# Kernel optimization log

Measured on AMD Instinct MI355X. Metric: run time of the kernel, lower is better.

## Reference

```python
import jax, jax.numpy as jnp
import numpy as np

B, N, DIM = 2, 2048, 1024
HEADS, DIM_HEAD = 16, 64
INNER = HEADS * DIM_HEAD  # 1024
SCALE = DIM_HEAD ** -0.5


def setup_inputs() -> dict:
    key = jax.random.key(0)
    ks = jax.random.split(key, 8)
    s = DIM ** -0.5
    return {
        "x1": jax.random.normal(ks[0], (B, N, DIM), jnp.float32),
        "x2": jax.random.normal(ks[1], (B, N, DIM), jnp.float32),
        "W_qkv1": jax.random.normal(ks[2], (DIM, INNER * 3), jnp.float32) * s,
        "W_qkv2": jax.random.normal(ks[3], (DIM, INNER * 3), jnp.float32) * s,
        "W_out1": jax.random.normal(ks[4], (INNER, DIM), jnp.float32) * s,
        "b_out1": jnp.zeros((DIM,), jnp.float32),
        "W_out2": jax.random.normal(ks[5], (INNER, DIM), jnp.float32) * s,
        "b_out2": jnp.zeros((DIM,), jnp.float32),
    }


def _split_heads(t):
    # [b, n, (h d)] -> [b, h, n, d]
    b, n, _ = t.shape
    return t.reshape(b, n, HEADS, DIM_HEAD).transpose(0, 2, 1, 3)


def _merge_heads(t):
    # [b, h, n, d] -> [b, n, (h d)]
    b, h, n, d = t.shape
    return t.transpose(0, 2, 1, 3).reshape(b, n, h * d)


def reference(x1, x2, W_qkv1, W_qkv2, W_out1, b_out1, W_out2, b_out2):
    qkv1 = x1 @ W_qkv1  # [b, n, 3*inner]
    qkv2 = x2 @ W_qkv2
    q1, k1, v1 = [_split_heads(t) for t in jnp.split(qkv1, 3, axis=-1)]
    q2, k2, v2 = [_split_heads(t) for t in jnp.split(qkv2, 3, axis=-1)]

    # direction 1: queries from stream 2 attend to keys/values of stream 1
    dots1 = jnp.einsum('bhid,bhjd->bhij', q2, k1) * SCALE
    attn1 = jax.nn.softmax(dots1, axis=-1)
    out1 = jnp.einsum('bhij,bhjd->bhid', attn1, v1)
    out1 = _merge_heads(out1) @ W_out1 + b_out1

    # direction 2: queries from stream 1 attend to keys/values of stream 2
    dots2 = jnp.einsum('bhid,bhjd->bhij', q1, k2) * SCALE
    attn2 = jax.nn.softmax(dots2, axis=-1)
    out2 = jnp.einsum('bhij,bhjd->bhid', attn2, v2)
    out2 = _merge_heads(out2) @ W_out2 + b_out2

    return (out1, out2)
```

## Files before the change

### kernel.cpp

```cpp
#include <hip/hip_runtime.h>

typedef __attribute__((ext_vector_type(8))) short short8;
typedef __attribute__((ext_vector_type(4))) float f32x4;
typedef __attribute__((ext_vector_type(16))) float f32x16;
using u16 = unsigned short;

#define DEV static __device__ __forceinline__
#define SCL 0.18033688011112042f

DEV u16 f2bf(float f) {
  union { float f; unsigned u; } v; v.f = f;
  unsigned r = v.u + 0x7FFFu + ((v.u >> 16) & 1u);
  return (u16)(r >> 16);
}

DEV unsigned cvtpk(float lo, float hi_) {
  unsigned d;
  asm("v_cvt_pk_bf16_f32 %0, %1, %2" : "=v"(d) : "v"(lo), "v"(hi_));
  return d;
}

DEV void gld16(const void* g, void* l) {
  __builtin_amdgcn_global_load_lds(
      (const __attribute__((address_space(1))) unsigned*)g,
      (__attribute__((address_space(3))) unsigned*)l, 16, 0, 0);
}

__global__ __launch_bounds__(256) void conv_f32_bf16(const float* __restrict__ s0,
                                                     const float* __restrict__ s1,
                                                     u16* __restrict__ d0,
                                                     u16* __restrict__ d1, int n8) {
  const float* src = blockIdx.z ? s1 : s0;
  u16* dst = blockIdx.z ? d1 : d0;
  int i = blockIdx.x * 256 + threadIdx.x;
  if (i >= n8) return;
  const float4* s = reinterpret_cast<const float4*>(src) + (size_t)i * 2;
  float4 a = s[0], b = s[1];
  union { u16 s[8]; uint4 v; } t;
  t.s[0]=f2bf(a.x); t.s[1]=f2bf(a.y); t.s[2]=f2bf(a.z); t.s[3]=f2bf(a.w);
  t.s[4]=f2bf(b.x); t.s[5]=f2bf(b.y); t.s[6]=f2bf(b.z); t.s[7]=f2bf(b.w);
  reinterpret_cast<uint4*>(dst)[i] = t.v;
}

__global__ __launch_bounds__(256) void transpose_w(const float* __restrict__ s0,
                                                   const float* __restrict__ s1,
                                                   u16* __restrict__ d0,
                                                   u16* __restrict__ d1, int R, int C,
                                                   int qcols, float qscale) {
  const float* src = blockIdx.z ? s1 : s0;
  u16* dst = blockIdx.z ? d1 : d0;
  __shared__ float tile[32][33];
  int tx = threadIdx.x & 31, ty = threadIdx.x >> 5;
  int rb = blockIdx.y * 32, cb = blockIdx.x * 32;
#pragma unroll
  for (int j = 0; j < 32; j += 8)
    tile[ty + j][tx] = src[(size_t)(rb + ty + j) * C + cb + tx];
  __syncthreads();
#pragma unroll
  for (int j = 0; j < 32; j += 8) {
    int c = cb + ty + j;
    float sc = (c < qcols) ? qscale : 1.0f;
    dst[(size_t)c * R + rb + tx] = f2bf(tile[tx][ty + j] * sc);
  }
}

__global__ __launch_bounds__(256) void gemm_bt(
    const u16* __restrict__ A0, const u16* __restrict__ A1,
    const u16* __restrict__ B0, const u16* __restrict__ B1,
    u16* __restrict__ Cb0, u16* __restrict__ Cb1,
    float* __restrict__ Cf0, float* __restrict__ Cf1,
    const float* __restrict__ bias0, const float* __restrict__ bias1,
    int M, int N, int K) {
  const int z = blockIdx.z;
  const u16* A  = z ? A1 : A0;
  const u16* Bt = z ? B1 : B0;
  u16* Cb = z ? Cb1 : Cb0;
  float* Cf = z ? Cf1 : Cf0;
  const float* bias = z ? bias1 : bias0;

  __shared__ __align__(16) char smem[32768];
  char* As = smem;
  char* Bs = smem + 16384;
  const int tid = threadIdx.x;
  const int lane = tid & 63, wave = tid >> 6;
  const int wm = wave >> 1, wn = wave & 1;
  const int lr = lane & 15, lk = lane >> 4;
  const size_t m0 = (size_t)blockIdx.x * 128, n0 = (size_t)blockIdx.y * 128;

  f32x4 acc[4][4] = {};

  for (int k0 = 0; k0 < K; k0 += 64) {
    __syncthreads();
#pragma unroll
    for (int i = 0; i < 4; ++i) {
      int idx = tid + i * 256;
      int r = idx >> 3, c = idx & 7;
      int cs = c ^ (r & 7);
      gld16(A + (m0 + r) * (size_t)K + k0 + cs * 8, As + idx * 16);
    }
#pragma unroll
    for (int i = 0; i < 4; ++i) {
      int idx = tid + i * 256;
      int r = idx >> 3, c = idx & 7;
      int cs = c ^ (r & 7);
      gld16(Bt + (n0 + r) * (size_t)K + k0 + cs * 8, Bs + idx * 16);
    }
    __syncthreads();
#pragma unroll
    for (int kk = 0; kk < 2; ++kk) {
      short8 af[4], bfr[4];
#pragma unroll
      for (int mf = 0; mf < 4; ++mf) {
        int r = wm * 64 + mf * 16 + lr;
        af[mf] = *reinterpret_cast<const short8*>(As + r * 128 + (((kk * 4 + lk) ^ (r & 7)) * 16));
      }
#pragma unroll
      for (int nf = 0; nf < 4; ++nf) {
        int r = wn * 64 + nf * 16 + lr;
        bfr[nf] = *reinterpret_cast<const short8*>(Bs + r * 128 + (((kk * 4 + lk) ^ (r & 7)) * 16));
      }
#pragma unroll
      for (int mf = 0; mf < 4; ++mf)
#pragma unroll
        for (int nf = 0; nf < 4; ++nf)
          acc[mf][nf] = __builtin_amdgcn_mfma_f32_16x16x32_bf16(af[mf], bfr[nf], acc[mf][nf], 0, 0, 0);
    }
  }
  const int row0 = (int)m0 + wm * 64, col0 = (int)n0 + wn * 64;
  if (Cf) {
#pragma unroll
    for (int nf = 0; nf < 4; ++nf) {
      int col = col0 + nf * 16 + lr;
      float bv = bias ? bias[col] : 0.0f;
#pragma unroll
      for (int mf = 0; mf < 4; ++mf)
#pragma unroll
        for (int g = 0; g < 4; ++g) {
          int row = row0 + mf * 16 + lk * 4 + g;
          Cf[(size_t)row * N + col] = acc[mf][nf][g] + bv;
        }
    }
  } else {
#pragma unroll
    for (int nf = 0; nf < 4; ++nf) {
      int col = col0 + nf * 16 + lr;
#pragma unroll
      for (int mf = 0; mf < 4; ++mf)
#pragma unroll
        for (int g = 0; g < 4; ++g) {
          int row = row0 + mf * 16 + lk * 4 + g;
          Cb[(size_t)row * N + col] = f2bf(acc[mf][nf][g]);
        }
    }
  }
}

__global__ __launch_bounds__(256) void vtrans(const u16* __restrict__ q0,
                                              const u16* __restrict__ q1,
                                              u16* __restrict__ v0p,
                                              u16* __restrict__ v1p) {
  const u16* qkv = blockIdx.z ? q1 : q0;
  u16* vT = blockIdx.z ? v1p : v0p;
  __shared__ u16 tile[64][72];
  int t = threadIdx.x;
  int bh = blockIdx.y;
  int b = bh >> 4, h = bh & 15;
  int n0 = blockIdx.x * 64;
  int n = t >> 2, dc = t & 3;
  const u16* src = qkv + (size_t)(b * 2048 + n0 + n) * 3072 + 2048 + h * 64 + dc * 16;
  uint4 w0 = *reinterpret_cast<const uint4*>(src);
  uint4 w1 = *reinterpret_cast<const uint4*>(src + 8);
  *reinterpret_cast<uint4*>(&tile[n][dc * 16]) = w0;
  *reinterpret_cast<uint4*>(&tile[n][dc * 16 + 8]) = w1;
  __syncthreads();
  int d = t >> 2, nc = t & 3;
  union { u16 s[8]; uint4 v; } o0, o1;
#pragma unroll
  for (int j = 0; j < 8; ++j) { o0.s[j] = tile[nc * 16 + j][d]; o1.s[j] = tile[nc * 16 + 8 + j][d]; }
  u16* dst = vT + ((size_t)(bh * 64 + d)) * 2048 + n0 + nc * 16;
  *reinterpret_cast<uint4*>(dst) = o0.v;
  *reinterpret_cast<uint4*>(dst + 8) = o1.v;
}

#define KOFF0 0
#define VOFF0 (8192 + 64)
#define KOFF1 (16384 + 128)
#define VOFF1 (KOFF1 + 8192 + 64)

__global__ __launch_bounds__(256, 2) void flash(
    const u16* __restrict__ qkv1, const u16* __restrict__ qkv2,
    const u16* __restrict__ vT1, const u16* __restrict__ vT2,
    u16* __restrict__ ao1, u16* __restrict__ ao2) {
  const int bid = blockIdx.x;
  const int bh_dir = bid & 63;
  const int qt = bid >> 6;
  const int dir = bh_dir >> 5;
  const int bh = bh_dir & 31;
  const int b = bh >> 4, h = bh & 15;
  const u16* qkvQ  = dir ? qkv1 : qkv2;
  const u16* qkvKV = dir ? qkv2 : qkv1;
  const u16* vT    = dir ? vT2 : vT1;
  u16* Oout        = dir ? ao2 : ao1;

  __shared__ __align__(16) char smem[33024];

  const int tid = threadIdx.x;
  const int lane = tid & 63, wave = tid >> 6;
  const int l31 = lane & 31, hi = lane >> 5;

  const int qbase = qt * 256 + wave * 64;
  const u16* qp0 = qkvQ + (size_t)(b * 2048 + qbase + l31) * 3072 + h * 64 + hi * 8;
  const u16* qp1 = qp0 + (size_t)32 * 3072;
  short8 qf0[4], qf1[4];
#pragma unroll
  for (int c = 0; c < 4; ++c) {
    qf0[c] = *reinterpret_cast<const short8*>(qp0 + c * 16);
    qf1[c] = *reinterpret_cast<const short8*>(qp1 + c * 16);
  }

  auto STAGE = [&](char* kb, char* vb, int kv0) {
#pragma unroll
    for (int i = 0; i < 2; ++i) {
      int idx = tid + i * 256;
      int r = idx >> 3, c = idx & 7, cs = c ^ (r & 7);
      gld16(qkvKV + (size_t)(b * 2048 + kv0 + r) * 3072 + 1024 + h * 64 + cs * 8, kb + idx * 16);
      gld16(vT + (size_t)(bh * 64 + r) * 2048 + kv0 + cs * 8, vb + idx * 16);
    }
  };

  short8 ones;
#pragma unroll
  for (int j = 0; j < 8; ++j) ones[j] = (short)0x3F80;

  f32x16 oA0 = {}, oA1 = {}, oB0 = {}, oB1 = {}, laccA = {}, laccB = {};

  STAGE(smem + KOFF0, smem + VOFF0, 0);

  union U8 { unsigned u[4]; short8 s8; };

  for (int t = 0; t < 32; ++t) {
    char* Ks = smem + ((t & 1) ? KOFF1 : KOFF0);
    char* Vs = smem + ((t & 1) ? VOFF1 : VOFF0);
    __syncthreads();
    if (t < 31)
      STAGE(smem + ((t & 1) ? KOFF0 : KOFF1), smem + ((t & 1) ? VOFF0 : VOFF1), (t + 1) * 64);

    short8 kf[8];
#pragma unroll
    for (int c = 0; c < 4; ++c) {
      int sw = ((c * 2 + hi) ^ (l31 & 7)) * 16;
      kf[c]     = *reinterpret_cast<const short8*>(Ks + l31 * 128 + sw);
      kf[c + 4] = *reinterpret_cast<const short8*>(Ks + (32 + l31) * 128 + sw);
    }

    f32x16 sA0 = {}, sA1 = {};
#pragma unroll
    for (int c = 0; c < 4; ++c) {
      sA0 = __builtin_amdgcn_mfma_f32_32x32x16_bf16(kf[c],     qf0[c], sA0, 0, 0, 0);
      sA1 = __builtin_amdgcn_mfma_f32_32x32x16_bf16(kf[c + 4], qf0[c], sA1, 0, 0, 0);
    }
#pragma unroll
    for (int r = 0; r < 16; ++r) sA0[r] = __builtin_exp2f(sA0[r]);
#pragma unroll
    for (int r = 0; r < 16; ++r) sA1[r] = __builtin_exp2f(sA1[r]);
    short8 paA[4];
#pragma unroll
    for (int kc = 0; kc < 4; ++kc) {
      const f32x16& S = (kc < 2) ? sA0 : sA1;
      int rb = (kc & 1) * 8;
      unsigned a0 = cvtpk(S[rb + 0], S[rb + 1]);
      unsigned b0 = cvtpk(S[rb + 4], S[rb + 5]);
      asm volatile("v_permlane32_swap_b32 %0, %1" : "+v"(a0), "+v"(b0));
      unsigned a1 = cvtpk(S[rb + 2], S[rb + 3]);
      unsigned b1 = cvtpk(S[rb + 6], S[rb + 7]);
      asm volatile("v_permlane32_swap_b32 %0, %1" : "+v"(a1), "+v"(b1));
      U8 u; u.u[0] = a0; u.u[1] = a1; u.u[2] = b0; u.u[3] = b1;
      paA[kc] = u.s8;
    }

    f32x16 sB0 = {}, sB1 = {};
#pragma unroll
    for (int c = 0; c < 4; ++c) {
      sB0 = __builtin_amdgcn_mfma_f32_32x32x16_bf16(kf[c],     qf1[c], sB0, 0, 0, 0);
      sB1 = __builtin_amdgcn_mfma_f32_32x32x16_bf16(kf[c + 4], qf1[c], sB1, 0, 0, 0);
    }

    short8 vf[8];
#pragma unroll
    for (int kc = 0; kc < 4; ++kc) {
      int sw = ((kc * 2 + hi) ^ (l31 & 7)) * 16;
      vf[kc]     = *reinterpret_cast<const short8*>(Vs + l31 * 128 + sw);
      vf[kc + 4] = *reinterpret_cast<const short8*>(Vs + (32 + l31) * 128 + sw);
    }

#pragma unroll
    for (int r = 0; r < 16; ++r) sB0[r] = __builtin_exp2f(sB0[r]);
#pragma unroll
    for (int r = 0; r < 16; ++r) sB1[r] = __builtin_exp2f(sB1[r]);
    short8 paB[4];
#pragma unroll
    for (int kc = 0; kc < 4; ++kc) {
      const f32x16& S = (kc < 2) ? sB0 : sB1;
      int rb = (kc & 1) * 8;
      unsigned a0 = cvtpk(S[rb + 0], S[rb + 1]);
      unsigned b0 = cvtpk(S[rb + 4], S[rb + 5]);
      asm volatile("v_permlane32_swap_b32 %0, %1" : "+v"(a0), "+v"(b0));
      unsigned a1 = cvtpk(S[rb + 2], S[rb + 3]);
      unsigned b1 = cvtpk(S[rb + 6], S[rb + 7]);
      asm volatile("v_permlane32_swap_b32 %0, %1" : "+v"(a1), "+v"(b1));
      U8 u; u.u[0] = a0; u.u[1] = a1; u.u[2] = b0; u.u[3] = b1;
      paB[kc] = u.s8;
    }

#pragma unroll
    for (int kc = 0; kc < 4; ++kc) {
      oA0 = __builtin_amdgcn_mfma_f32_32x32x16_bf16(paA[kc], vf[kc],     oA0, 0, 0, 0);
      oA1 = __builtin_amdgcn_mfma_f32_32x32x16_bf16(paA[kc], vf[kc + 4], oA1, 0, 0, 0);
      oB0 = __builtin_amdgcn_mfma_f32_32x32x16_bf16(paB[kc], vf[kc],     oB0, 0, 0, 0);
      oB1 = __builtin_amdgcn_mfma_f32_32x32x16_bf16(paB[kc], vf[kc + 4], oB1, 0, 0, 0);
      laccA = __builtin_amdgcn_mfma_f32_32x32x16_bf16(paA[kc], ones, laccA, 0, 0, 0);
      laccB = __builtin_amdgcn_mfma_f32_32x32x16_bf16(paB[kc], ones, laccB, 0, 0, 0);
    }
  }

  const int rowbase = b * 2048 + qt * 256 + wave * 64;
#pragma unroll
  for (int r = 0; r < 16; ++r) {
    int q = (r & 3) + 8 * (r >> 2) + 4 * hi;
    float liA = 1.0f / laccA[r], liB = 1.0f / laccB[r];
    u16* opA = Oout + (size_t)(rowbase + q) * 1024 + h * 64 + l31;
    u16* opB = opA + (size_t)32 * 1024;
    opA[0]  = f2bf(oA0[r] * liA);
    opA[32] = f2bf(oA1[r] * liA);
    opB[0]  = f2bf(oB0[r] * liB);
    opB[32] = f2bf(oB1[r] * liB);
  }
}

extern "C" void kernel_launch(void* const* d_in, const int* in_sizes, int n_in,
                              void* d_out, int out_size, void* d_ws, size_t ws_size,
                              hipStream_t stream) {
  const float* x1  = (const float*)d_in[0];
  const float* x2  = (const float*)d_in[1];
  const float* Wq1 = (const float*)d_in[2];
  const float* Wq2 = (const float*)d_in[3];
  const float* Wo1 = (const float*)d_in[4];
  const float* bo1 = (const float*)d_in[5];
  const float* Wo2 = (const float*)d_in[6];
  const float* bo2 = (const float*)d_in[7];
  float* out = (float*)d_out;

  char* ws = (char*)d_ws;
  u16* x1b  = (u16*)(ws + 0);
  u16* x2b  = (u16*)(ws + 8388608);
  u16* Wq1t = (u16*)(ws + 16777216);
  u16* Wq2t = (u16*)(ws + 23068672);
  u16* Wo1t = (u16*)(ws + 29360128);
  u16* Wo2t = (u16*)(ws + 31457280);
  u16* qkv1 = (u16*)(ws + 33554432);
  u16* qkv2 = (u16*)(ws + 58720256);
  u16* vT1  = (u16*)(ws + 83886080);
  u16* vT2  = (u16*)(ws + 92274688);
  u16* ao1  = (u16*)(ws + 100663296);
  u16* ao2  = (u16*)(ws + 109051904);

  conv_f32_bf16<<<dim3(2048, 1, 2), 256, 0, stream>>>(x1, x2, x1b, x2b, 4194304 / 8);
  transpose_w<<<dim3(96, 32, 2), 256, 0, stream>>>(Wq1, Wq2, Wq1t, Wq2t, 1024, 3072,
                                                   1024, SCL);
  transpose_w<<<dim3(32, 32, 2), 256, 0, stream>>>(Wo1, Wo2, Wo1t, Wo2t, 1024, 1024,
                                                   0, 1.0f);

  gemm_bt<<<dim3(32, 24, 2), 256, 0, stream>>>(x1b, x2b, Wq1t, Wq2t, qkv1, qkv2,
                                               nullptr, nullptr, nullptr, nullptr,
                                               4096, 3072, 1024);

  vtrans<<<dim3(32, 32, 2), 256, 0, stream>>>(qkv1, qkv2, vT1, vT2);

  flash<<<dim3(512), 256, 0, stream>>>(qkv1, qkv2, vT1, vT2, ao1, ao2);

  gemm_bt<<<dim3(32, 8, 2), 256, 0, stream>>>(ao1, ao2, Wo1t, Wo2t, nullptr, nullptr,
                                              out, out + 4194304, bo1, bo2,
                                              4096, 1024, 1024);
}
```

Baseline: 211.3 us.

## Fuse QKV GEMM with V transpose via 256x256 ping-pong tiled kernel

Replaces the 128x128 QKV projection GEMM and the separate V-transpose kernel with a new 256x256-tile, 512-thread GEMM. It double-buffers K-tiles in 128KB of dynamic LDS, interleaves global-to-LDS staging with MFMA phases under explicit barriers and priority hints, remaps block IDs across XCDs, and writes the V columns directly in transposed layout. The flash kernel is also reordered to issue both query-half S MFMAs first, load V earlier, and raise wave priority around MFMA bursts. The large LDS footprint limits occupancy and the manual barrier schedule is fragile.

```diff
diff --git a/kernel.cpp b/kernel.cpp
--- a/kernel.cpp
+++ b/kernel.cpp
@@ -64,17 +64,169 @@
   }
 }
 
+extern __shared__ char dsmem[];
+
+__global__ __launch_bounds__(512, 2) void gemm256(
+    const u16* __restrict__ A0, const u16* __restrict__ A1,
+    const u16* __restrict__ B0, const u16* __restrict__ B1,
+    u16* __restrict__ Q0, u16* __restrict__ Q1,
+    u16* __restrict__ V0, u16* __restrict__ V1) {
+  const int orig = blockIdx.x;
+  const int wgid = (orig & 7) * 48 + (orig >> 3);
+  const int z = wgid / 192, rr_ = wgid % 192;
+  const int bx = rr_ / 12, by = rr_ % 12;
+  const u16* Ag = z ? A1 : A0;
+  const u16* Bg = z ? B1 : B0;
+  const size_t m0 = (size_t)bx * 256, n0 = (size_t)by * 256;
+  const int K = 1024;
+
+  const int tid = threadIdx.x;
+  const int lane = tid & 63;
+  const int wave = tid >> 6;
+  const int wm = wave >> 2, wn = wave & 3;
+  const int lr = lane & 15, lk = lane >> 4;
+
+  f32x4 acc[8][4] = {};
+
+  auto STG = [&](int buf, int kt, int opi) {
+    int idx = opi * 512 + tid;
+    char* base = dsmem + buf * 65536;
+    if (idx < 2048) {
+      int r = idx >> 3, c = idx & 7;
+      gld16(Ag + (m0 + r) * (size_t)K + kt * 64 + ((c ^ (r & 7)) * 8), base + idx * 16);
+    } else {
+      int j = idx - 2048;
+      int r = j >> 3, c = j & 7;
+      gld16(Bg + (n0 + r) * (size_t)K + kt * 64 + ((c ^ (r & 7)) * 8), base + 32768 + j * 16);
+    }
+  };
+  auto DSA = [&](short8* af, int buf, int mg, int kh) {
+#pragma unroll
+    for (int i = 0; i < 4; ++i) {
+      int row = wm * 128 + (mg * 4 + i) * 16 + lr;
+      af[i] = *reinterpret_cast<const short8*>(
+          dsmem + buf * 65536 + row * 128 + (((kh * 4 + lk) ^ (row & 7)) * 16));
+    }
+  };
+  auto DSB = [&](short8* bf_, int buf, int kh) {
+#pragma unroll
+    for (int j = 0; j < 4; ++j) {
+      int row = wn * 64 + j * 16 + lr;
+      bf_[j] = *reinterpret_cast<const short8*>(
+          dsmem + buf * 65536 + 32768 + row * 128 + (((kh * 4 + lk) ^ (row & 7)) * 16));
+    }
+  };
+
+#pragma unroll
+  for (int o = 0; o < 8; ++o) STG(0, 0, o);
+  asm volatile("s_waitcnt vmcnt(0)" ::: "memory");
+  __syncthreads();
+
+  int cur = 0;
+  for (int kt = 0; kt < 16; ++kt) {
+    short8 af[4], bf_[4];
+    const int more = (kt < 15);
+
+    DSA(af, cur, 0, 0); DSB(bf_, cur, 0);
+    if (more) { STG(cur ^ 1, kt + 1, 0); STG(cur ^ 1, kt + 1, 1);
+                STG(cur ^ 1, kt + 1, 2); STG(cur ^ 1, kt + 1, 3); }
+    __builtin_amdgcn_s_barrier();
+    asm volatile("s_waitcnt lgkmcnt(0)" ::: "memory");
+    __builtin_amdgcn_sched_barrier(0);
+    __builtin_amdgcn_s_setprio(1);
+#pragma unroll
+    for (int i = 0; i < 4; ++i)
+#pragma unroll
+      for (int j = 0; j < 4; ++j)
+        acc[i][j] = __builtin_amdgcn_mfma_f32_16x16x32_bf16(af[i], bf_[j], acc[i][j], 0, 0, 0);
+    __builtin_amdgcn_s_setprio(0);
+    __builtin_amdgcn_s_barrier();
+
+    DSA(af, cur, 1, 0);
+    if (more) { STG(cur ^ 1, kt + 1, 4); STG(cur ^ 1, kt + 1, 5); }
+    __builtin_amdgcn_s_barrier();
+    asm volatile("s_waitcnt lgkmcnt(0)" ::: "memory");
+    __builtin_amdgcn_sched_barrier(0);
+    __builtin_amdgcn_s_setprio(1);
+#pragma unroll
+    for (int i = 0; i < 4; ++i)
+#pragma unroll
+      for (int j = 0; j < 4; ++j)
+        acc[4 + i][j] = __builtin_amdgcn_mfma_f32_16x16x32_bf16(af[i], bf_[j], acc[4 + i][j], 0, 0, 0);
+    __builtin_amdgcn_s_setprio(0);
+    __builtin_amdgcn_s_barrier();
+
+    DSA(af, cur, 0, 1); DSB(bf_, cur, 1);
+    if (more) { STG(cur ^ 1, kt + 1, 6); STG(cur ^ 1, kt + 1, 7); }
+    __builtin_amdgcn_s_barrier();
+    asm volatile("s_waitcnt lgkmcnt(0)" ::: "memory");
+    __builtin_amdgcn_sched_barrier(0);
+    __builtin_amdgcn_s_setprio(1);
+#pragma unroll
+    for (int i = 0; i < 4; ++i)
+#pragma unroll
+      for (int j = 0; j < 4; ++j)
+        acc[i][j] = __builtin_amdgcn_mfma_f32_16x16x32_bf16(af[i], bf_[j], acc[i][j], 0, 0, 0);
+    __builtin_amdgcn_s_setprio(0);
+    __builtin_amdgcn_s_barrier();
+
+    DSA(af, cur, 1, 1);
+    __builtin_amdgcn_s_barrier();
+    asm volatile("s_waitcnt lgkmcnt(0)" ::: "memory");
+    __builtin_amdgcn_sched_barrier(0);
+    __builtin_amdgcn_s_setprio(1);
+#pragma unroll
+    for (int i = 0; i < 4; ++i)
+#pragma unroll
+      for (int j = 0; j < 4; ++j)
+        acc[4 + i][j] = __builtin_amdgcn_mfma_f32_16x16x32_bf16(af[i], bf_[j], acc[4 + i][j], 0, 0, 0);
+    __builtin_amdgcn_s_setprio(0);
+    asm volatile("s_waitcnt vmcnt(0)" ::: "memory");
+    __builtin_amdgcn_s_barrier();
+    cur ^= 1;
+  }
+
+  const int row0 = (int)m0 + wm * 128;
+  const int col0 = (int)n0 + wn * 64;
+  u16* Qo = z ? Q1 : Q0;
+  u16* Vo = z ? V1 : V0;
+  if (col0 < 2048) {
+#pragma unroll
+    for (int mf = 0; mf < 8; ++mf)
+#pragma unroll
+      for (int nf = 0; nf < 4; ++nf) {
+        int col = col0 + nf * 16 + lr;
+#pragma unroll
+        for (int g = 0; g < 4; ++g) {
+          int row = row0 + mf * 16 + lk * 4 + g;
+          Qo[(size_t)row * 3072 + col] = f2bf(acc[mf][nf][g]);
+        }
+      }
+  } else {
+#pragma unroll
+    for (int mf = 0; mf < 8; ++mf)
+#pragma unroll
+      for (int nf = 0; nf < 4; ++nf) {
+        int col = col0 + nf * 16 + lr;
+        int row = row0 + mf * 16 + lk * 4;
+        size_t vbase = ((size_t)((row >> 11) * 1024 + (col - 2048))) * 2048 + (row & 2047);
+        union { u16 s[4]; unsigned long long v; } pk;
+#pragma unroll
+        for (int g = 0; g < 4; ++g) pk.s[g] = f2bf(acc[mf][nf][g]);
+        *reinterpret_cast<unsigned long long*>(Vo + vbase) = pk.v;
+      }
+  }
+}
+
 __global__ __launch_bounds__(256) void gemm_bt(
     const u16* __restrict__ A0, const u16* __restrict__ A1,
     const u16* __restrict__ B0, const u16* __restrict__ B1,
-    u16* __restrict__ Cb0, u16* __restrict__ Cb1,
     float* __restrict__ Cf0, float* __restrict__ Cf1,
     const float* __restrict__ bias0, const float* __restrict__ bias1,
     int M, int N, int K) {
   const int z = blockIdx.z;
   const u16* A  = z ? A1 : A0;
   const u16* Bt = z ? B1 : B0;
-  u16* Cb = z ? Cb1 : Cb0;
   float* Cf = z ? Cf1 : Cf0;
   const float* bias = z ? bias1 : bias0;
 
@@ -127,59 +279,18 @@
     }
   }
   const int row0 = (int)m0 + wm * 64, col0 = (int)n0 + wn * 64;
-  if (Cf) {
-#pragma unroll
-    for (int nf = 0; nf < 4; ++nf) {
-      int col = col0 + nf * 16 + lr;
-      float bv = bias ? bias[col] : 0.0f;
-#pragma unroll
-      for (int mf = 0; mf < 4; ++mf)
-#pragma unroll
-        for (int g = 0; g < 4; ++g) {
-          int row = row0 + mf * 16 + lk * 4 + g;
-          Cf[(size_t)row * N + col] = acc[mf][nf][g] + bv;
-        }
-    }
-  } else {
-#pragma unroll
-    for (int nf = 0; nf < 4; ++nf) {
-      int col = col0 + nf * 16 + lr;
-#pragma unroll
-      for (int mf = 0; mf < 4; ++mf)
-#pragma unroll
-        for (int g = 0; g < 4; ++g) {
-          int row = row0 + mf * 16 + lk * 4 + g;
-          Cb[(size_t)row * N + col] = f2bf(acc[mf][nf][g]);
-        }
-    }
-  }
-}
-
-__global__ __launch_bounds__(256) void vtrans(const u16* __restrict__ q0,
-                                              const u16* __restrict__ q1,
-                                              u16* __restrict__ v0p,
-                                              u16* __restrict__ v1p) {
-  const u16* qkv = blockIdx.z ? q1 : q0;
-  u16* vT = blockIdx.z ? v1p : v0p;
-  __shared__ u16 tile[64][72];
-  int t = threadIdx.x;
-  int bh = blockIdx.y;
-  int b = bh >> 4, h = bh & 15;
-  int n0 = blockIdx.x * 64;
-  int n = t >> 2, dc = t & 3;
-  const u16* src = qkv + (size_t)(b * 2048 + n0 + n) * 3072 + 2048 + h * 64 + dc * 16;
-  uint4 w0 = *reinterpret_cast<const uint4*>(src);
-  uint4 w1 = *reinterpret_cast<const uint4*>(src + 8);
-  *reinterpret_cast<uint4*>(&tile[n][dc * 16]) = w0;
-  *reinterpret_cast<uint4*>(&tile[n][dc * 16 + 8]) = w1;
-  __syncthreads();
-  int d = t >> 2, nc = t & 3;
-  union { u16 s[8]; uint4 v; } o0, o1;
-#pragma unroll
-  for (int j = 0; j < 8; ++j) { o0.s[j] = tile[nc * 16 + j][d]; o1.s[j] = tile[nc * 16 + 8 + j][d]; }
-  u16* dst = vT + ((size_t)(bh * 64 + d)) * 2048 + n0 + nc * 16;
-  *reinterpret_cast<uint4*>(dst) = o0.v;
-  *reinterpret_cast<uint4*>(dst + 8) = o1.v;
+#pragma unroll
+  for (int nf = 0; nf < 4; ++nf) {
+    int col = col0 + nf * 16 + lr;
+    float bv = bias[col];
+#pragma unroll
+    for (int mf = 0; mf < 4; ++mf)
+#pragma unroll
+      for (int g = 0; g < 4; ++g) {
+        int row = row0 + mf * 16 + lk * 4 + g;
+        Cf[(size_t)row * N + col] = acc[mf][nf][g] + bv;
+      }
+  }
 }
 
 #define KOFF0 0
@@ -253,12 +364,25 @@
       kf[c + 4] = *reinterpret_cast<const short8*>(Ks + (32 + l31) * 128 + sw);
     }
 
-    f32x16 sA0 = {}, sA1 = {};
+    f32x16 sA0 = {}, sA1 = {}, sB0 = {}, sB1 = {};
+    __builtin_amdgcn_s_setprio(1);
 #pragma unroll
     for (int c = 0; c < 4; ++c) {
       sA0 = __builtin_amdgcn_mfma_f32_32x32x16_bf16(kf[c],     qf0[c], sA0, 0, 0, 0);
       sA1 = __builtin_amdgcn_mfma_f32_32x32x16_bf16(kf[c + 4], qf0[c], sA1, 0, 0, 0);
-    }
+      sB0 = __builtin_amdgcn_mfma_f32_32x32x16_bf16(kf[c],     qf1[c], sB0, 0, 0, 0);
+      sB1 = __builtin_amdgcn_mfma_f32_32x32x16_bf16(kf[c + 4], qf1[c], sB1, 0, 0, 0);
+    }
+    __builtin_amdgcn_s_setprio(0);
+
+    short8 vf[8];
+#pragma unroll
+    for (int kc = 0; kc < 4; ++kc) {
+      int sw = ((kc * 2 + hi) ^ (l31 & 7)) * 16;
+      vf[kc]     = *reinterpret_cast<const short8*>(Vs + l31 * 128 + sw);
+      vf[kc + 4] = *reinterpret_cast<const short8*>(Vs + (32 + l31) * 128 + sw);
+    }
+
 #pragma unroll
     for (int r = 0; r < 16; ++r) sA0[r] = __builtin_exp2f(sA0[r]);
 #pragma unroll
@@ -277,21 +401,14 @@
       U8 u; u.u[0] = a0; u.u[1] = a1; u.u[2] = b0; u.u[3] = b1;
       paA[kc] = u.s8;
     }
-
-    f32x16 sB0 = {}, sB1 = {};
-#pragma unroll
-    for (int c = 0; c < 4; ++c) {
-      sB0 = __builtin_amdgcn_mfma_f32_32x32x16_bf16(kf[c],     qf1[c], sB0, 0, 0, 0);
-      sB1 = __builtin_amdgcn_mfma_f32_32x32x16_bf16(kf[c + 4], qf1[c], sB1, 0, 0, 0);
-    }
-
-    short8 vf[8];
+    __builtin_amdgcn_s_setprio(1);
 #pragma unroll
     for (int kc = 0; kc < 4; ++kc) {
-      int sw = ((kc * 2 + hi) ^ (l31 & 7)) * 16;
-      vf[kc]     = *reinterpret_cast<const short8*>(Vs + l31 * 128 + sw);
-      vf[kc + 4] = *reinterpret_cast<const short8*>(Vs + (32 + l31) * 128 + sw);
-    }
+      oA0 = __builtin_amdgcn_mfma_f32_32x32x16_bf16(paA[kc], vf[kc],     oA0, 0, 0, 0);
+      oA1 = __builtin_amdgcn_mfma_f32_32x32x16_bf16(paA[kc], vf[kc + 4], oA1, 0, 0, 0);
+      laccA = __builtin_amdgcn_mfma_f32_32x32x16_bf16(paA[kc], ones, laccA, 0, 0, 0);
+    }
+    __builtin_amdgcn_s_setprio(0);
 
 #pragma unroll
     for (int r = 0; r < 16; ++r) sB0[r] = __builtin_exp2f(sB0[r]);
@@ -311,16 +428,14 @@
       U8 u; u.u[0] = a0; u.u[1] = a1; u.u[2] = b0; u.u[3] = b1;
       paB[kc] = u.s8;
     }
-
+    __builtin_amdgcn_s_setprio(1);
 #pragma unroll
     for (int kc = 0; kc < 4; ++kc) {
-      oA0 = __builtin_amdgcn_mfma_f32_32x32x16_bf16(paA[kc], vf[kc],     oA0, 0, 0, 0);
-      oA1 = __builtin_amdgcn_mfma_f32_32x32x16_bf16(paA[kc], vf[kc + 4], oA1, 0, 0, 0);
       oB0 = __builtin_amdgcn_mfma_f32_32x32x16_bf16(paB[kc], vf[kc],     oB0, 0, 0, 0);
       oB1 = __builtin_amdgcn_mfma_f32_32x32x16_bf16(paB[kc], vf[kc + 4], oB1, 0, 0, 0);
-      laccA = __builtin_amdgcn_mfma_f32_32x32x16_bf16(paA[kc], ones, laccA, 0, 0, 0);
       laccB = __builtin_amdgcn_mfma_f32_32x32x16_bf16(paB[kc], ones, laccB, 0, 0, 0);
     }
+    __builtin_amdgcn_s_setprio(0);
   }
 
   const int rowbase = b * 2048 + qt * 256 + wave * 64;
@@ -364,21 +479,21 @@
   u16* ao1  = (u16*)(ws + 100663296);
   u16* ao2  = (u16*)(ws + 109051904);
 
+  hipFuncSetAttribute(reinterpret_cast<const void*>(gemm256),
+                      hipFuncAttributeMaxDynamicSharedMemorySize, 131072);
+
   conv_f32_bf16<<<dim3(2048, 1, 2), 256, 0, stream>>>(x1, x2, x1b, x2b, 4194304 / 8);
   transpose_w<<<dim3(96, 32, 2), 256, 0, stream>>>(Wq1, Wq2, Wq1t, Wq2t, 1024, 3072,
                                                    1024, SCL);
   transpose_w<<<dim3(32, 32, 2), 256, 0, stream>>>(Wo1, Wo2, Wo1t, Wo2t, 1024, 1024,
                                                    0, 1.0f);
 
-  gemm_bt<<<dim3(32, 24, 2), 256, 0, stream>>>(x1b, x2b, Wq1t, Wq2t, qkv1, qkv2,
-                                               nullptr, nullptr, nullptr, nullptr,
-                                               4096, 3072, 1024);
-
-  vtrans<<<dim3(32, 32, 2), 256, 0, stream>>>(qkv1, qkv2, vT1, vT2);
+  gemm256<<<dim3(384), 512, 131072, stream>>>(x1b, x2b, Wq1t, Wq2t,
+                                              qkv1, qkv2, vT1, vT2);
 
   flash<<<dim3(512), 256, 0, stream>>>(qkv1, qkv2, vT1, vT2, ao1, ao2);
 
-  gemm_bt<<<dim3(32, 8, 2), 256, 0, stream>>>(ao1, ao2, Wo1t, Wo2t, nullptr, nullptr,
+  gemm_bt<<<dim3(32, 8, 2), 256, 0, stream>>>(ao1, ao2, Wo1t, Wo2t,
                                               out, out + 4194304, bo1, bo2,
                                               4096, 1024, 1024);
 }
```

Result: slower. 222.0 us (+5.0%).
